# Kernel tuning notes

Measured on AMD Instinct MI355X. Metric: run time of the kernel, lower is better.

Reference implementation:

```python
import jax, jax.numpy as jnp
import numpy as np

NEG_LARGE = -2.0**32 + 1.0


def setup_inputs() -> dict:
    key = jax.random.key(0)
    ks = jax.random.split(key, 8)
    B, L, D = 2048, 200, 64  # D = embedding_dim, features are 2D wide
    H1, H2 = 80, 40
    queries = jax.random.normal(ks[0], (B, 2 * D), dtype=jnp.float32)
    user_behaviors = jax.random.normal(ks[1], (B, L, 2 * D), dtype=jnp.float32)
    masks = jax.random.randint(ks[2], (B, L), 0, 2, dtype=jnp.int32)
    s = 1.0 / np.sqrt(8 * D)
    w1 = jax.random.uniform(ks[3], (8 * D, H1), minval=-s, maxval=s, dtype=jnp.float32)
    b1 = jnp.zeros((H1,), jnp.float32)
    s2 = 1.0 / np.sqrt(H1)
    w2 = jax.random.uniform(ks[4], (H1, H2), minval=-s2, maxval=s2, dtype=jnp.float32)
    b2 = jnp.zeros((H2,), jnp.float32)
    s3 = 1.0 / np.sqrt(H2)
    w3 = jax.random.uniform(ks[5], (H2, 1), minval=-s3, maxval=s3, dtype=jnp.float32)
    b3 = jnp.zeros((1,), jnp.float32)
    return {"queries": queries, "user_behaviors": user_behaviors, "masks": masks,
            "w1": w1, "b1": b1, "w2": w2, "b2": b2, "w3": w3, "b3": b3}


def reference(queries, user_behaviors, masks, w1, b1, w2, b2, w3, b3):
    B, L, twoD = user_behaviors.shape
    q = jnp.broadcast_to(queries[:, None, :], (B, L, twoD))  # (B, L, 2D)
    feats = jnp.concatenate([q, user_behaviors, q - user_behaviors,
                             q * user_behaviors], axis=-1)  # (B, L, 8D)
    h = jax.nn.sigmoid(jnp.einsum('blf,fh->blh', feats, w1) + b1)
    h = jax.nn.sigmoid(jnp.einsum('blh,hk->blk', h, w2) + b2)
    scores = jnp.einsum('blk,ko->blo', h, w3) + b3  # (B, L, 1)
    valid = (masks != 0)[:, :, None]
    scores = jnp.where(valid, scores, NEG_LARGE)
    attn = jax.nn.softmax(scores, axis=1)  # (B, L, 1)
    return jnp.sum(attn * user_behaviors, axis=1)  # (B, 2D)
```

## Files before the change

### kernel.cpp

```cpp
#include <hip/hip_runtime.h>
#include <cstddef>


#define L_   200
#define D2_  128

typedef __attribute__((ext_vector_type(8))) short bf16x8;
typedef __attribute__((ext_vector_type(4))) float f32x4;
typedef __attribute__((ext_vector_type(4))) unsigned int u32x4;

union U8 { u32x4 u; bf16x8 b; };

__device__ __forceinline__ float sigmoidf_(float x) { return 1.0f / (1.0f + __expf(-x)); }

__device__ __forceinline__ unsigned int f2bf_(float x) {
  unsigned int u = __float_as_uint(x);
  return (u + 0x7fffu + ((u >> 16) & 1u)) >> 16;
}
__device__ __forceinline__ unsigned int pk2_(float a, float b) {
  return f2bf_(a) | (f2bf_(b) << 16);
}
__device__ __forceinline__ unsigned int pk2f_(float a, float b) {
  unsigned int r;
  asm("v_cvt_pk_bf16_f32 %0, %1, %2" : "=v"(r) : "v"(a), "v"(b));
  return r;
}

extern "C" __global__ void __launch_bounds__(128)
din_setup_kernel(const float* __restrict__ queries,
                 const float* __restrict__ w1,
                 const float* __restrict__ b1,
                 const float* __restrict__ w2,
                 float* __restrict__ qt,
                 float* __restrict__ wbc,
                 float* __restrict__ wd,
                 u32x4* __restrict__ w2a,
                 u32x4* __restrict__ w2b)
{
  const int bb = blockIdx.x;
  const int t  = threadIdx.x;

  if (bb < 8) {
    for (int s = bb * 160 + t; s < bb * 160 + 160; s += 128) {
      int nn = s & 15, kg = (s >> 4) & 3, g = s >> 6;
      int kc = g / 5, nt = g - kc * 5;
      int h = nt * 16 + nn, k0 = kc * 32 + kg * 8;
      #pragma unroll
      for (int j = 0; j < 8; ++j) {
        int k = k0 + j;
        wbc[s * 8 + j] = w1[(128 + k) * 80 + h] - w1[(256 + k) * 80 + h];
        wd [s * 8 + j] = w1[(384 + k) * 80 + h];
      }
    }
  } else if (bb == 8) {
    for (int s = t; s < 384; s += 128) {
      int nn = s & 15, g = s >> 4, nt2 = g >> 3, kg = g & 7;
      int j = nt2 * 16 + nn, k0 = kg * 8;
      u32x4 v = { 0u, 0u, 0u, 0u };
      if (j < 40) {
        float e0 = w2[(k0 + 0) * 40 + j], e1 = w2[(k0 + 1) * 40 + j];
        float e2 = w2[(k0 + 2) * 40 + j], e3 = w2[(k0 + 3) * 40 + j];
        float e4 = w2[(k0 + 4) * 40 + j], e5 = w2[(k0 + 5) * 40 + j];
        float e6 = w2[(k0 + 6) * 40 + j], e7 = w2[(k0 + 7) * 40 + j];
        v = (u32x4){ pk2_(e0, e1), pk2_(e2, e3), pk2_(e4, e5), pk2_(e6, e7) };
      }
      w2a[s] = v;
    }
    for (int s = t; s < 96; s += 128) {
      int nn = s & 15, g = s >> 4, nt2 = g >> 1, kgt = g & 1;
      int j = nt2 * 16 + nn, k0 = 64 + kgt * 8;
      u32x4 v = { 0u, 0u, 0u, 0u };
      if (j < 40) {
        float e0 = w2[(k0 + 0) * 40 + j], e1 = w2[(k0 + 1) * 40 + j];
        float e2 = w2[(k0 + 2) * 40 + j], e3 = w2[(k0 + 3) * 40 + j];
        float e4 = w2[(k0 + 4) * 40 + j], e5 = w2[(k0 + 5) * 40 + j];
        float e6 = w2[(k0 + 6) * 40 + j], e7 = w2[(k0 + 7) * 40 + j];
        v = (u32x4){ pk2_(e0, e1), pk2_(e2, e3), pk2_(e4, e5), pk2_(e6, e7) };
      }
      w2b[s] = v;
    }
  } else {
    const int b = bb - 9;
    __shared__ float qs[128];
    if (t < 128) qs[t] = queries[(size_t)b * D2_ + t];
    __syncthreads();
    if (t < 80) {
      float acc = b1[t];
      #pragma unroll 4
      for (int k = 0; k < 128; ++k)
        acc += qs[k] * (w1[k * 80 + t] + w1[(256 + k) * 80 + t]);
      qt[(size_t)b * 80 + t] = acc;
    }
  }
}

extern "C" __global__ void __launch_bounds__(256, 4)
din_scores_kernel(const float* __restrict__ queries,
                  const float* __restrict__ ub,
                  const float* __restrict__ b2,
                  const float* __restrict__ w3,
                  const float* __restrict__ qt,
                  const float* __restrict__ wbc,
                  const float* __restrict__ wd,
                  const u32x4* __restrict__ w2a,
                  const u32x4* __restrict__ w2b,
                  float* __restrict__ scores_ws)
{
  __shared__ __align__(16) char  pool[20480];
  __shared__ __align__(16) char  scratch[10240];
  __shared__ __align__(16) float qt_s[80];
  __shared__ __align__(16) float b2_s[48];
  __shared__ __align__(16) float w3_s[48];

  const int bc    = blockIdx.x;
  const int b     = bc >> 1;
  const int chunk = bc & 1;
  const int t     = threadIdx.x;
  const int wave  = t >> 6;
  const int lane  = t & 63;
  const int n16   = lane & 15;
  const int rg    = lane >> 4;

  const int st  = chunk ? (wave < 2 ? 7 + wave * 2 : 9 + wave) : wave * 2;
  const int cnt = chunk ? (wave < 2 ? 2 : 1) : (wave < 3 ? 2 : 1);

  const float* ubbase = ub + (size_t)b * (L_ * D2_);
  const float* qrow   = queries + (size_t)b * D2_;

  if (t < 80) qt_s[t] = qt[(size_t)b * 80 + t];
  if (t < 48) {
    b2_s[t] = (t < 40) ? b2[t] : 0.0f;
    w3_s[t] = (t < 40) ? w3[t] : 0.0f;
  }

  {
    u32x4* dst = (u32x4*)pool;
    const float4* wbc4 = (const float4*)wbc;
    const float4* wd4  = (const float4*)wd;
    #pragma unroll
    for (int i = 0; i < 5; ++i) {
      int s = i * 256 + t;
      int kg = (s >> 4) & 3, g = s >> 6;
      int kc = g / 5;
      int k0 = kc * 32 + kg * 8;
      float4 c0 = wbc4[2 * s], c1 = wbc4[2 * s + 1];
      float4 d0 = wd4 [2 * s], d1 = wd4 [2 * s + 1];
      float4 q0 = *(const float4*)(qrow + k0);
      float4 q1 = *(const float4*)(qrow + k0 + 4);
      dst[s] = (u32x4){ pk2f_(c0.x + q0.x * d0.x, c0.y + q0.y * d0.y),
                        pk2f_(c0.z + q0.z * d0.z, c0.w + q0.w * d0.w),
                        pk2f_(c1.x + q1.x * d1.x, c1.y + q1.y * d1.y),
                        pk2f_(c1.z + q1.z * d1.z, c1.w + q1.w * d1.w) };
    }
  }
  __syncthreads();

  const float* pa[2];
  #pragma unroll
  for (int i = 0; i < 2; ++i) {
    int row = (st + i) * 16 + n16;
    int rc  = (row < L_) ? row : (L_ - 1);
    pa[i] = ubbase + (size_t)rc * D2_ + rg * 8;
  }

  f32x4 acc[2][5];
  #pragma unroll
  for (int i = 0; i < 2; ++i)
    #pragma unroll
    for (int nt = 0; nt < 5; ++nt) acc[i][nt] = (f32x4){0.f, 0.f, 0.f, 0.f};

  const bf16x8* Bf = (const bf16x8*)pool;
  for (int kc = 0; kc < 4; ++kc) {
    U8 av[2];
    #pragma unroll
    for (int i = 0; i < 2; ++i) {
      if (i < cnt) {
        const float4* src = (const float4*)(pa[i] + kc * 32);
        float4 u0 = src[0], u1 = src[1];
        av[i].u = (u32x4){ pk2f_(u0.x, u0.y), pk2f_(u0.z, u0.w),
                           pk2f_(u1.x, u1.y), pk2f_(u1.z, u1.w) };
      }
    }
    #pragma unroll
    for (int nt = 0; nt < 5; ++nt) {
      bf16x8 bv = Bf[(kc * 5 + nt) * 64 + lane];
      #pragma unroll
      for (int i = 0; i < 2; ++i)
        if (i < cnt)
          acc[i][nt] = __builtin_amdgcn_mfma_f32_16x16x32_bf16(av[i].b, bv, acc[i][nt], 0, 0, 0);
    }
  }

  {
    unsigned short* hv  = (unsigned short*)(scratch + wave * 2560);
    const bf16x8*   hvf = (const bf16x8*)(scratch + wave * 2560);
    const bf16x8*   w2af = (const bf16x8*)w2a;
    const bf16x8*   w2bf = (const bf16x8*)w2b;

    for (int i = 0; i < 2; ++i) {
      if (i < cnt) {
        const int mt = st + i;

        #pragma unroll
        for (int nt = 0; nt < 5; ++nt) {
          int h  = nt * 16 + n16;
          int kg = h >> 3;
          float qtv = qt_s[h];
          #pragma unroll
          for (int r = 0; r < 4; ++r) {
            float x = acc[i][nt][r] + qtv;
            hv[(kg * 16 + rg * 4 + r) * 8 + (h & 7)] = (unsigned short)f2bf_(sigmoidf_(x));
          }
        }

        f32x4 acc2[3];
        #pragma unroll
        for (int n2 = 0; n2 < 3; ++n2) acc2[n2] = (f32x4){0.f, 0.f, 0.f, 0.f};

        #pragma unroll
        for (int ks = 0; ks < 2; ++ks) {
          bf16x8 av = hvf[(ks * 4 + rg) * 16 + n16];
          #pragma unroll
          for (int n2 = 0; n2 < 3; ++n2) {
            bf16x8 bv = w2af[(n2 * 8 + ks * 4 + rg) * 16 + n16];
            acc2[n2] = __builtin_amdgcn_mfma_f32_16x16x32_bf16(av, bv, acc2[n2], 0, 0, 0);
          }
        }
        {
          bf16x8 av = (bf16x8){0, 0, 0, 0, 0, 0, 0, 0};
          if (lane < 32) av = hvf[(8 + rg) * 16 + n16];
          #pragma unroll
          for (int n2 = 0; n2 < 3; ++n2) {
            bf16x8 bv = (bf16x8){0, 0, 0, 0, 0, 0, 0, 0};
            if (lane < 32) bv = w2bf[(n2 * 2 + rg) * 16 + n16];
            acc2[n2] = __builtin_amdgcn_mfma_f32_16x16x32_bf16(av, bv, acc2[n2], 0, 0, 0);
          }
        }

        #pragma unroll
        for (int r = 0; r < 4; ++r) {
          float s = 0.0f;
          #pragma unroll
          for (int n2 = 0; n2 < 3; ++n2) {
            int j = n2 * 16 + n16;
            s += sigmoidf_(acc2[n2][r] + b2_s[j]) * w3_s[j];
          }
          s += __shfl_xor(s, 1, 64);
          s += __shfl_xor(s, 2, 64);
          s += __shfl_xor(s, 4, 64);
          s += __shfl_xor(s, 8, 64);
          int l = mt * 16 + rg * 4 + r;
          if (n16 == 0 && l < L_) scores_ws[(size_t)b * L_ + l] = s;
        }
      }
    }
  }
}

extern "C" __global__ void __launch_bounds__(256, 4)
din_softmax_wsum_kernel(const float* __restrict__ ub,
                        const int*   __restrict__ masks,
                        const float* __restrict__ scores_ws,
                        float* __restrict__ out)
{
  __shared__ __align__(16) float scores_s[208];
  __shared__ __align__(16) float wsum_s[1088];
  __shared__ float red_s[8];

  const int b    = blockIdx.x;
  const int t    = threadIdx.x;
  const int wave = t >> 6;
  const int lane = t & 63;

  const float* ubbase = ub + (size_t)b * (L_ * D2_);

  float sval = -INFINITY;
  if (t < L_) {
    int   mv = masks[(size_t)b * L_ + t];
    float sc = scores_ws[(size_t)b * L_ + t];
    sval = mv ? sc : -4294967295.0f;
  }
  float m = sval;
  #pragma unroll
  for (int o = 32; o > 0; o >>= 1) m = fmaxf(m, __shfl_xor(m, o, 64));
  if (lane == 0) red_s[wave] = m;
  __syncthreads();
  m = fmaxf(fmaxf(red_s[0], red_s[1]), fmaxf(red_s[2], red_s[3]));
  float e = (t < L_) ? __expf(sval - m) : 0.0f;
  float ssum = e;
  #pragma unroll
  for (int o = 32; o > 0; o >>= 1) ssum += __shfl_xor(ssum, o, 64);
  if (lane == 0) red_s[4 + wave] = ssum;
  __syncthreads();
  ssum = red_s[4] + red_s[5] + red_s[6] + red_s[7];
  if (t < L_) scores_s[t] = e / ssum;
  __syncthreads();

  {
    const float4* ub4base = (const float4*)ubbase;
    int d4 = t & 31;
    int lg = t >> 5;
    float4 o = make_float4(0.f, 0.f, 0.f, 0.f);
    #pragma unroll
    for (int l = lg; l < L_; l += 8) {
      float w = scores_s[l];
      float4 v = ub4base[l * 32 + d4];
      o.x += w * v.x; o.y += w * v.y; o.z += w * v.z; o.w += w * v.w;
    }
    *(float4*)(wsum_s + lg * 136 + d4 * 4) = o;
    __syncthreads();
    if (t < 128) {
      float s = 0.0f;
      #pragma unroll
      for (int g = 0; g < 8; ++g) s += wsum_s[g * 136 + t];
      out[(size_t)b * 128 + t] = s;
    }
  }
}

extern "C" __global__ void __launch_bounds__(256, 4)
din_attn_fallback(const float* __restrict__ queries,
                  const float* __restrict__ ub,
                  const int*   __restrict__ masks,
                  const float* __restrict__ b2,
                  const float* __restrict__ w3,
                  const float* __restrict__ qt,
                  const float* __restrict__ wbc,
                  const float* __restrict__ wd,
                  const u32x4* __restrict__ w2a,
                  const u32x4* __restrict__ w2b,
                  float* __restrict__ out)
{
  __shared__ __align__(16) char  pool[33280];
  __shared__ __align__(16) float wsum_s[1088];
  __shared__ __align__(16) float qt_s[80];
  __shared__ __align__(16) float b2_s[48];
  __shared__ __align__(16) float w3_s[48];
  __shared__ __align__(16) float scores_s[208];
  __shared__ float red_s[8];

  const int b    = blockIdx.x;
  const int t    = threadIdx.x;
  const int wave = t >> 6;
  const int lane = t & 63;
  const int n16  = lane & 15;
  const int rg   = lane >> 4;

  const float* ubbase = ub + (size_t)b * (L_ * D2_);
  const float* qrow   = queries + (size_t)b * D2_;

  if (t < 80) qt_s[t] = qt[(size_t)b * 80 + t];
  if (t < 48) {
    b2_s[t] = (t < 40) ? b2[t] : 0.0f;
    w3_s[t] = (t < 40) ? w3[t] : 0.0f;
  }

  {
    u32x4* dst = (u32x4*)pool;
    const float4* wbc4 = (const float4*)wbc;
    const float4* wd4  = (const float4*)wd;
    #pragma unroll
    for (int i = 0; i < 5; ++i) {
      int s = i * 256 + t;
      int kg = (s >> 4) & 3, g = s >> 6;
      int kc = g / 5;
      int k0 = kc * 32 + kg * 8;
      float4 c0 = wbc4[2 * s], c1 = wbc4[2 * s + 1];
      float4 d0 = wd4 [2 * s], d1 = wd4 [2 * s + 1];
      float4 q0 = *(const float4*)(qrow + k0);
      float4 q1 = *(const float4*)(qrow + k0 + 4);
      dst[s] = (u32x4){ pk2f_(c0.x + q0.x * d0.x, c0.y + q0.y * d0.y),
                        pk2f_(c0.z + q0.z * d0.z, c0.w + q0.w * d0.w),
                        pk2f_(c1.x + q1.x * d1.x, c1.y + q1.y * d1.y),
                        pk2f_(c1.z + q1.z * d1.z, c1.w + q1.w * d1.w) };
    }
  }
  __syncthreads();

  f32x4 acc[4][5];
  #pragma unroll
  for (int i = 0; i < 4; ++i)
    #pragma unroll
    for (int nt = 0; nt < 5; ++nt) acc[i][nt] = (f32x4){0.f, 0.f, 0.f, 0.f};

  const bf16x8* Bf = (const bf16x8*)pool;
  for (int kc = 0; kc < 4; ++kc) {
    bf16x8 bvv[5];
    #pragma unroll
    for (int nt = 0; nt < 5; ++nt) bvv[nt] = Bf[(kc * 5 + nt) * 64 + lane];
    #pragma unroll
    for (int i = 0; i < 4; ++i) {
      int mt = wave + i * 4;
      if (mt < 13) {
        int row = mt * 16 + n16;
        float4 u0 = make_float4(0.f, 0.f, 0.f, 0.f);
        float4 u1 = make_float4(0.f, 0.f, 0.f, 0.f);
        if (row < L_) {
          const float4* src = (const float4*)(ubbase + (size_t)row * D2_ + kc * 32 + rg * 8);
          u0 = src[0]; u1 = src[1];
        }
        U8 av;
        av.u = (u32x4){ pk2f_(u0.x, u0.y), pk2f_(u0.z, u0.w),
                        pk2f_(u1.x, u1.y), pk2f_(u1.z, u1.w) };
        #pragma unroll
        for (int nt = 0; nt < 5; ++nt)
          acc[i][nt] = __builtin_amdgcn_mfma_f32_16x16x32_bf16(av.b, bvv[nt], acc[i][nt], 0, 0, 0);
      }
    }
  }
  __syncthreads();

  {
    unsigned short* hv = (unsigned short*)pool;
    #pragma unroll
    for (int i = 0; i < 4; ++i) {
      int mt = wave + i * 4;
      if (mt < 13) {
        #pragma unroll
        for (int nt = 0; nt < 5; ++nt) {
          int h = nt * 16 + n16;
          float qtv = qt_s[h];
          int kg = h >> 3;
          int slotbase = (kg < 8) ? (mt * 8 + kg) : (1664 + mt * 2 + (kg - 8));
          #pragma unroll
          for (int r = 0; r < 4; ++r) {
            float x = acc[i][nt][r] + qtv;
            hv[(slotbase * 16 + rg * 4 + r) * 8 + (h & 7)] =
                (unsigned short)f2bf_(sigmoidf_(x));
          }
        }
      }
    }
  }

  {
    const bf16x8* hvf  = (const bf16x8*)pool;
    const bf16x8* w2af = (const bf16x8*)w2a;
    const bf16x8* w2bf = (const bf16x8*)w2b;
    #pragma unroll
    for (int i = 0; i < 4; ++i) {
      int mt = wave + i * 4;
      if (mt < 13) {
        f32x4 acc2[3];
        #pragma unroll
        for (int n2 = 0; n2 < 3; ++n2) acc2[n2] = (f32x4){0.f, 0.f, 0.f, 0.f};
        #pragma unroll
        for (int ks = 0; ks < 2; ++ks) {
          bf16x8 av = hvf[(mt * 8 + ks * 4 + rg) * 16 + n16];
          #pragma unroll
          for (int n2 = 0; n2 < 3; ++n2) {
            bf16x8 bv = w2af[(n2 * 8 + ks * 4 + rg) * 16 + n16];
            acc2[n2] = __builtin_amdgcn_mfma_f32_16x16x32_bf16(av, bv, acc2[n2], 0, 0, 0);
          }
        }
        {
          bf16x8 av = (bf16x8){0, 0, 0, 0, 0, 0, 0, 0};
          if (lane < 32) av = hvf[(1664 + mt * 2 + rg) * 16 + n16];
          #pragma unroll
          for (int n2 = 0; n2 < 3; ++n2) {
            bf16x8 bv = (bf16x8){0, 0, 0, 0, 0, 0, 0, 0};
            if (lane < 32) bv = w2bf[(n2 * 2 + rg) * 16 + n16];
            acc2[n2] = __builtin_amdgcn_mfma_f32_16x16x32_bf16(av, bv, acc2[n2], 0, 0, 0);
          }
        }
        #pragma unroll
        for (int r = 0; r < 4; ++r) {
          float s = 0.0f;
          #pragma unroll
          for (int n2 = 0; n2 < 3; ++n2) {
            int j = n2 * 16 + n16;
            s += sigmoidf_(acc2[n2][r] + b2_s[j]) * w3_s[j];
          }
          s += __shfl_xor(s, 1, 64);
          s += __shfl_xor(s, 2, 64);
          s += __shfl_xor(s, 4, 64);
          s += __shfl_xor(s, 8, 64);
          int l = mt * 16 + rg * 4 + r;
          if (n16 == 0 && l < L_) scores_s[l] = s;
        }
      }
    }
  }
  __syncthreads();

  float sval = -INFINITY;
  if (t < L_) {
    int mv = masks[(size_t)b * L_ + t];
    sval = mv ? scores_s[t] : -4294967295.0f;
  }
  float m = sval;
  #pragma unroll
  for (int o = 32; o > 0; o >>= 1) m = fmaxf(m, __shfl_xor(m, o, 64));
  if (lane == 0) red_s[wave] = m;
  __syncthreads();
  m = fmaxf(fmaxf(red_s[0], red_s[1]), fmaxf(red_s[2], red_s[3]));
  float e = (t < L_) ? __expf(sval - m) : 0.0f;
  float ssum = e;
  #pragma unroll
  for (int o = 32; o > 0; o >>= 1) ssum += __shfl_xor(ssum, o, 64);
  if (lane == 0) red_s[4 + wave] = ssum;
  __syncthreads();
  ssum = red_s[4] + red_s[5] + red_s[6] + red_s[7];
  if (t < L_) scores_s[t] = e / ssum;
  __syncthreads();

  {
    const float4* ub4base = (const float4*)ubbase;
    int d4 = t & 31;
    int lg = t >> 5;
    float4 o = make_float4(0.f, 0.f, 0.f, 0.f);
    #pragma unroll
    for (int l = lg; l < L_; l += 8) {
      float w = scores_s[l];
      float4 v = ub4base[l * 32 + d4];
      o.x += w * v.x; o.y += w * v.y; o.z += w * v.z; o.w += w * v.w;
    }
    *(float4*)(wsum_s + lg * 136 + d4 * 4) = o;
    __syncthreads();
    if (t < 128) {
      float s = 0.0f;
      #pragma unroll
      for (int g = 0; g < 8; ++g) s += wsum_s[g * 136 + t];
      out[(size_t)b * 128 + t] = s;
    }
  }
}

extern "C" void kernel_launch(void* const* d_in, const int* in_sizes, int n_in,
                              void* d_out, int out_size, void* d_ws, size_t ws_size,
                              hipStream_t stream) {
  const float* queries = (const float*)d_in[0];
  const float* ub      = (const float*)d_in[1];
  const int*   masks   = (const int*)d_in[2];
  const float* w1      = (const float*)d_in[3];
  const float* b1      = (const float*)d_in[4];
  const float* w2      = (const float*)d_in[5];
  const float* b2      = (const float*)d_in[6];
  const float* w3      = (const float*)d_in[7];
  float* out = (float*)d_out;

  const int B = in_sizes[0] / D2_;

  char*  ws  = (char*)d_ws;
  float* qt  = (float*)ws;
  float* wbc = (float*)(ws + (size_t)B * 320);
  float* wd  = (float*)(ws + (size_t)B * 320 + 40960);
  u32x4* w2a = (u32x4*)(ws + (size_t)B * 320 + 81920);
  u32x4* w2b = (u32x4*)(ws + (size_t)B * 320 + 88064);
  size_t sc_off = (size_t)B * 320 + 90112;
  float* scores = (float*)(ws + sc_off);
  size_t need = sc_off + (size_t)B * L_ * 4;

  din_setup_kernel<<<B + 9, 128, 0, stream>>>(queries, w1, b1, w2, qt, wbc, wd, w2a, w2b);

  if (ws_size >= need) {
    din_scores_kernel<<<2 * B, 256, 0, stream>>>(queries, ub, b2, w3,
                                                 qt, wbc, wd, w2a, w2b, scores);
    din_softmax_wsum_kernel<<<B, 256, 0, stream>>>(ub, masks, scores, out);
  } else {
    din_attn_fallback<<<B, 256, 0, stream>>>(queries, ub, masks, b2, w3,
                                             qt, wbc, wd, w2a, w2b, out);
  }
}
```

Before: 375.0 us.

## Precompute per-batch bf16 query-folded W1 in setup kernel, read from global in scores

The setup kernel now builds, for each batch row, the query-dependent bf16 B-matrix for the first layer (W_b - W_c + q*W_d) in the MFMA fragment layout and writes it to workspace. The scores kernel loads those fragments straight from global instead of rebuilding them in LDS. It also keeps qt, b2 and w3 in registers rather than shared memory, which removes the LDS staging and the block barrier. The cost is about 20 KB of extra workspace writes and reads per batch row, plus heavier per-row work in the setup kernel.

Result: slower. 408.8 us (+9.0%).

```diff
diff --git a/kernel.cpp b/kernel.cpp
--- a/kernel.cpp
+++ b/kernel.cpp
@@ -24,6 +24,279 @@
   unsigned int r;
   asm("v_cvt_pk_bf16_f32 %0, %1, %2" : "=v"(r) : "v"(a), "v"(b));
   return r;
+}
+
+extern "C" __global__ void __launch_bounds__(256)
+din_setup2_kernel(const float* __restrict__ queries,
+                  const float* __restrict__ w1,
+                  const float* __restrict__ b1,
+                  const float* __restrict__ w2,
+                  float* __restrict__ qt,
+                  u32x4* __restrict__ w2a,
+                  u32x4* __restrict__ w2b,
+                  u32x4* __restrict__ bwq)
+{
+  const int bb = blockIdx.x;
+  const int t  = threadIdx.x;
+
+  if (bb == (int)gridDim.x - 1) {
+    for (int s = t; s < 384; s += 256) {
+      int nn = s & 15, g = s >> 4, nt2 = g >> 3, kg = g & 7;
+      int j = nt2 * 16 + nn, k0 = kg * 8;
+      u32x4 v = { 0u, 0u, 0u, 0u };
+      if (j < 40) {
+        float e0 = w2[(k0 + 0) * 40 + j], e1 = w2[(k0 + 1) * 40 + j];
+        float e2 = w2[(k0 + 2) * 40 + j], e3 = w2[(k0 + 3) * 40 + j];
+        float e4 = w2[(k0 + 4) * 40 + j], e5 = w2[(k0 + 5) * 40 + j];
+        float e6 = w2[(k0 + 6) * 40 + j], e7 = w2[(k0 + 7) * 40 + j];
+        v = (u32x4){ pk2_(e0, e1), pk2_(e2, e3), pk2_(e4, e5), pk2_(e6, e7) };
+      }
+      w2a[s] = v;
+    }
+    for (int s = t; s < 96; s += 256) {
+      int nn = s & 15, g = s >> 4, nt2 = g >> 1, kgt = g & 1;
+      int j = nt2 * 16 + nn, k0 = 64 + kgt * 8;
+      u32x4 v = { 0u, 0u, 0u, 0u };
+      if (j < 40) {
+        float e0 = w2[(k0 + 0) * 40 + j], e1 = w2[(k0 + 1) * 40 + j];
+        float e2 = w2[(k0 + 2) * 40 + j], e3 = w2[(k0 + 3) * 40 + j];
+        float e4 = w2[(k0 + 4) * 40 + j], e5 = w2[(k0 + 5) * 40 + j];
+        float e6 = w2[(k0 + 6) * 40 + j], e7 = w2[(k0 + 7) * 40 + j];
+        v = (u32x4){ pk2_(e0, e1), pk2_(e2, e3), pk2_(e4, e5), pk2_(e6, e7) };
+      }
+      w2b[s] = v;
+    }
+    return;
+  }
+
+  const int b = bb;
+  __shared__ float qs[128];
+  if (t < 128) qs[t] = queries[(size_t)b * D2_ + t];
+  __syncthreads();
+
+  if (t < 80) {
+    float acc = b1[t];
+    #pragma unroll 4
+    for (int k = 0; k < 128; ++k)
+      acc += qs[k] * (w1[k * 80 + t] + w1[(256 + k) * 80 + t]);
+    qt[(size_t)b * 80 + t] = acc;
+  }
+
+  u32x4* dst = bwq + (size_t)b * 1280;
+  #pragma unroll
+  for (int i = 0; i < 5; ++i) {
+    int s = i * 256 + t;
+    int nn = s & 15, kg = (s >> 4) & 3, g = s >> 6;
+    int kc = g / 5, nt = g - kc * 5;
+    int h = nt * 16 + nn, k0 = kc * 32 + kg * 8;
+    float wv[8];
+    #pragma unroll
+    for (int j = 0; j < 8; ++j) {
+      int k = k0 + j;
+      wv[j] = (w1[(128 + k) * 80 + h] - w1[(256 + k) * 80 + h])
+            + qs[k] * w1[(384 + k) * 80 + h];
+    }
+    dst[s] = (u32x4){ pk2f_(wv[0], wv[1]), pk2f_(wv[2], wv[3]),
+                      pk2f_(wv[4], wv[5]), pk2f_(wv[6], wv[7]) };
+  }
+}
+
+extern "C" __global__ void __launch_bounds__(256, 4)
+din_scores2_kernel(const float* __restrict__ ub,
+                   const float* __restrict__ b2,
+                   const float* __restrict__ w3,
+                   const float* __restrict__ qt,
+                   const u32x4* __restrict__ bwq,
+                   const u32x4* __restrict__ w2a,
+                   const u32x4* __restrict__ w2b,
+                   float* __restrict__ scores_ws)
+{
+  __shared__ __align__(16) char scratch[10240];
+
+  const int bc    = blockIdx.x;
+  const int b     = bc >> 1;
+  const int chunk = bc & 1;
+  const int t     = threadIdx.x;
+  const int wave  = t >> 6;
+  const int lane  = t & 63;
+  const int n16   = lane & 15;
+  const int rg    = lane >> 4;
+
+  const int st  = chunk ? (wave < 2 ? 7 + wave * 2 : 9 + wave) : wave * 2;
+  const int cnt = chunk ? (wave < 2 ? 2 : 1) : (wave < 3 ? 2 : 1);
+
+  const float* ubbase = ub + (size_t)b * (L_ * D2_);
+
+  float qtv[5], b2v[3], w3v[3];
+  #pragma unroll
+  for (int nt = 0; nt < 5; ++nt) qtv[nt] = qt[(size_t)b * 80 + nt * 16 + n16];
+  #pragma unroll
+  for (int n2 = 0; n2 < 3; ++n2) {
+    int j = n2 * 16 + n16;
+    int jc = (j < 40) ? j : 0;
+    b2v[n2] = b2[jc];
+    w3v[n2] = (j < 40) ? w3[jc] : 0.0f;
+  }
+
+  const float* pa[2];
+  #pragma unroll
+  for (int i = 0; i < 2; ++i) {
+    int row = (st + i) * 16 + n16;
+    int rc  = (row < L_) ? row : (L_ - 1);
+    pa[i] = ubbase + (size_t)rc * D2_ + rg * 8;
+  }
+
+  f32x4 acc[2][5];
+  #pragma unroll
+  for (int i = 0; i < 2; ++i)
+    #pragma unroll
+    for (int nt = 0; nt < 5; ++nt) acc[i][nt] = (f32x4){0.f, 0.f, 0.f, 0.f};
+
+  const u32x4* bq = bwq + (size_t)b * 1280;
+  for (int kc = 0; kc < 4; ++kc) {
+    U8 av[2];
+    #pragma unroll
+    for (int i = 0; i < 2; ++i) {
+      if (i < cnt) {
+        const float4* src = (const float4*)(pa[i] + kc * 32);
+        float4 u0 = src[0], u1 = src[1];
+        av[i].u = (u32x4){ pk2f_(u0.x, u0.y), pk2f_(u0.z, u0.w),
+                           pk2f_(u1.x, u1.y), pk2f_(u1.z, u1.w) };
+      }
+    }
+    #pragma unroll
+    for (int nt = 0; nt < 5; ++nt) {
+      U8 bv;
+      bv.u = bq[(kc * 5 + nt) * 64 + lane];
+      #pragma unroll
+      for (int i = 0; i < 2; ++i)
+        if (i < cnt)
+          acc[i][nt] = __builtin_amdgcn_mfma_f32_16x16x32_bf16(av[i].b, bv.b, acc[i][nt], 0, 0, 0);
+    }
+  }
+
+  {
+    unsigned short* hv  = (unsigned short*)(scratch + wave * 2560);
+    const bf16x8*   hvf = (const bf16x8*)(scratch + wave * 2560);
+    const bf16x8*   w2af = (const bf16x8*)w2a;
+    const bf16x8*   w2bf = (const bf16x8*)w2b;
+
+    for (int i = 0; i < 2; ++i) {
+      if (i < cnt) {
+        const int mt = st + i;
+
+        #pragma unroll
+        for (int nt = 0; nt < 5; ++nt) {
+          int h  = nt * 16 + n16;
+          int kg = h >> 3;
+          #pragma unroll
+          for (int r = 0; r < 4; ++r) {
+            float x = acc[i][nt][r] + qtv[nt];
+            hv[(kg * 16 + rg * 4 + r) * 8 + (h & 7)] = (unsigned short)f2bf_(sigmoidf_(x));
+          }
+        }
+
+        f32x4 acc2[3];
+        #pragma unroll
+        for (int n2 = 0; n2 < 3; ++n2) acc2[n2] = (f32x4){0.f, 0.f, 0.f, 0.f};
+
+        #pragma unroll
+        for (int ks = 0; ks < 2; ++ks) {
+          bf16x8 av = hvf[(ks * 4 + rg) * 16 + n16];
+          #pragma unroll
+          for (int n2 = 0; n2 < 3; ++n2) {
+            bf16x8 bv = w2af[(n2 * 8 + ks * 4 + rg) * 16 + n16];
+            acc2[n2] = __builtin_amdgcn_mfma_f32_16x16x32_bf16(av, bv, acc2[n2], 0, 0, 0);
+          }
+        }
+        {
+          bf16x8 av = (bf16x8){0, 0, 0, 0, 0, 0, 0, 0};
+          if (lane < 32) av = hvf[(8 + rg) * 16 + n16];
+          #pragma unroll
+          for (int n2 = 0; n2 < 3; ++n2) {
+            bf16x8 bv = (bf16x8){0, 0, 0, 0, 0, 0, 0, 0};
+            if (lane < 32) bv = w2bf[(n2 * 2 + rg) * 16 + n16];
+            acc2[n2] = __builtin_amdgcn_mfma_f32_16x16x32_bf16(av, bv, acc2[n2], 0, 0, 0);
+          }
+        }
+
+        #pragma unroll
+        for (int r = 0; r < 4; ++r) {
+          float s = 0.0f;
+          #pragma unroll
+          for (int n2 = 0; n2 < 3; ++n2)
+            s += sigmoidf_(acc2[n2][r] + b2v[n2]) * w3v[n2];
+          s += __shfl_xor(s, 1, 64);
+          s += __shfl_xor(s, 2, 64);
+          s += __shfl_xor(s, 4, 64);
+          s += __shfl_xor(s, 8, 64);
+          int l = mt * 16 + rg * 4 + r;
+          if (n16 == 0 && l < L_) scores_ws[(size_t)b * L_ + l] = s;
+        }
+      }
+    }
+  }
+}
+
+extern "C" __global__ void __launch_bounds__(256, 4)
+din_softmax_wsum_kernel(const float* __restrict__ ub,
+                        const int*   __restrict__ masks,
+                        const float* __restrict__ scores_ws,
+                        float* __restrict__ out)
+{
+  __shared__ __align__(16) float scores_s[208];
+  __shared__ __align__(16) float wsum_s[1088];
+  __shared__ float red_s[8];
+
+  const int b    = blockIdx.x;
+  const int t    = threadIdx.x;
+  const int wave = t >> 6;
+  const int lane = t & 63;
+
+  const float* ubbase = ub + (size_t)b * (L_ * D2_);
+
+  float sval = -INFINITY;
+  if (t < L_) {
+    int   mv = masks[(size_t)b * L_ + t];
+    float sc = scores_ws[(size_t)b * L_ + t];
+    sval = mv ? sc : -4294967295.0f;
+  }
+  float m = sval;
+  #pragma unroll
+  for (int o = 32; o > 0; o >>= 1) m = fmaxf(m, __shfl_xor(m, o, 64));
+  if (lane == 0) red_s[wave] = m;
+  __syncthreads();
+  m = fmaxf(fmaxf(red_s[0], red_s[1]), fmaxf(red_s[2], red_s[3]));
+  float e = (t < L_) ? __expf(sval - m) : 0.0f;
+  float ssum = e;
+  #pragma unroll
+  for (int o = 32; o > 0; o >>= 1) ssum += __shfl_xor(ssum, o, 64);
+  if (lane == 0) red_s[4 + wave] = ssum;
+  __syncthreads();
+  ssum = red_s[4] + red_s[5] + red_s[6] + red_s[7];
+  if (t < L_) scores_s[t] = e / ssum;
+  __syncthreads();
+
+  {
+    const float4* ub4base = (const float4*)ubbase;
+    int d4 = t & 31;
+    int lg = t >> 5;
+    float4 o = make_float4(0.f, 0.f, 0.f, 0.f);
+    #pragma unroll
+    for (int l = lg; l < L_; l += 8) {
+      float w = scores_s[l];
+      float4 v = ub4base[l * 32 + d4];
+      o.x += w * v.x; o.y += w * v.y; o.z += w * v.z; o.w += w * v.w;
+    }
+    *(float4*)(wsum_s + lg * 136 + d4 * 4) = o;
+    __syncthreads();
+    if (t < 128) {
+      float s = 0.0f;
+      #pragma unroll
+      for (int g = 0; g < 8; ++g) s += wsum_s[g * 136 + t];
+      out[(size_t)b * 128 + t] = s;
+    }
+  }
 }
 
 extern "C" __global__ void __launch_bounds__(128)
@@ -90,230 +363,6 @@
       for (int k = 0; k < 128; ++k)
         acc += qs[k] * (w1[k * 80 + t] + w1[(256 + k) * 80 + t]);
       qt[(size_t)b * 80 + t] = acc;
-    }
-  }
-}
-
-extern "C" __global__ void __launch_bounds__(256, 4)
-din_scores_kernel(const float* __restrict__ queries,
-                  const float* __restrict__ ub,
-                  const float* __restrict__ b2,
-                  const float* __restrict__ w3,
-                  const float* __restrict__ qt,
-                  const float* __restrict__ wbc,
-                  const float* __restrict__ wd,
-                  const u32x4* __restrict__ w2a,
-                  const u32x4* __restrict__ w2b,
-                  float* __restrict__ scores_ws)
-{
-  __shared__ __align__(16) char  pool[20480];
-  __shared__ __align__(16) char  scratch[10240];
-  __shared__ __align__(16) float qt_s[80];
-  __shared__ __align__(16) float b2_s[48];
-  __shared__ __align__(16) float w3_s[48];
-
-  const int bc    = blockIdx.x;
-  const int b     = bc >> 1;
-  const int chunk = bc & 1;
-  const int t     = threadIdx.x;
-  const int wave  = t >> 6;
-  const int lane  = t & 63;
-  const int n16   = lane & 15;
-  const int rg    = lane >> 4;
-
-  const int st  = chunk ? (wave < 2 ? 7 + wave * 2 : 9 + wave) : wave * 2;
-  const int cnt = chunk ? (wave < 2 ? 2 : 1) : (wave < 3 ? 2 : 1);
-
-  const float* ubbase = ub + (size_t)b * (L_ * D2_);
-  const float* qrow   = queries + (size_t)b * D2_;
-
-  if (t < 80) qt_s[t] = qt[(size_t)b * 80 + t];
-  if (t < 48) {
-    b2_s[t] = (t < 40) ? b2[t] : 0.0f;
-    w3_s[t] = (t < 40) ? w3[t] : 0.0f;
-  }
-
-  {
-    u32x4* dst = (u32x4*)pool;
-    const float4* wbc4 = (const float4*)wbc;
-    const float4* wd4  = (const float4*)wd;
-    #pragma unroll
-    for (int i = 0; i < 5; ++i) {
-      int s = i * 256 + t;
-      int kg = (s >> 4) & 3, g = s >> 6;
-      int kc = g / 5;
-      int k0 = kc * 32 + kg * 8;
-      float4 c0 = wbc4[2 * s], c1 = wbc4[2 * s + 1];
-      float4 d0 = wd4 [2 * s], d1 = wd4 [2 * s + 1];
-      float4 q0 = *(const float4*)(qrow + k0);
-      float4 q1 = *(const float4*)(qrow + k0 + 4);
-      dst[s] = (u32x4){ pk2f_(c0.x + q0.x * d0.x, c0.y + q0.y * d0.y),
-                        pk2f_(c0.z + q0.z * d0.z, c0.w + q0.w * d0.w),
-                        pk2f_(c1.x + q1.x * d1.x, c1.y + q1.y * d1.y),
-                        pk2f_(c1.z + q1.z * d1.z, c1.w + q1.w * d1.w) };
-    }
-  }
-  __syncthreads();
-
-  const float* pa[2];
-  #pragma unroll
-  for (int i = 0; i < 2; ++i) {
-    int row = (st + i) * 16 + n16;
-    int rc  = (row < L_) ? row : (L_ - 1);
-    pa[i] = ubbase + (size_t)rc * D2_ + rg * 8;
-  }
-
-  f32x4 acc[2][5];
-  #pragma unroll
-  for (int i = 0; i < 2; ++i)
-    #pragma unroll
-    for (int nt = 0; nt < 5; ++nt) acc[i][nt] = (f32x4){0.f, 0.f, 0.f, 0.f};
-
-  const bf16x8* Bf = (const bf16x8*)pool;
-  for (int kc = 0; kc < 4; ++kc) {
-    U8 av[2];
-    #pragma unroll
-    for (int i = 0; i < 2; ++i) {
-      if (i < cnt) {
-        const float4* src = (const float4*)(pa[i] + kc * 32);
-        float4 u0 = src[0], u1 = src[1];
-        av[i].u = (u32x4){ pk2f_(u0.x, u0.y), pk2f_(u0.z, u0.w),
-                           pk2f_(u1.x, u1.y), pk2f_(u1.z, u1.w) };
-      }
-    }
-    #pragma unroll
-    for (int nt = 0; nt < 5; ++nt) {
-      bf16x8 bv = Bf[(kc * 5 + nt) * 64 + lane];
-      #pragma unroll
-      for (int i = 0; i < 2; ++i)
-        if (i < cnt)
-          acc[i][nt] = __builtin_amdgcn_mfma_f32_16x16x32_bf16(av[i].b, bv, acc[i][nt], 0, 0, 0);
-    }
-  }
-
-  {
-    unsigned short* hv  = (unsigned short*)(scratch + wave * 2560);
-    const bf16x8*   hvf = (const bf16x8*)(scratch + wave * 2560);
-    const bf16x8*   w2af = (const bf16x8*)w2a;
-    const bf16x8*   w2bf = (const bf16x8*)w2b;
-
-    for (int i = 0; i < 2; ++i) {
-      if (i < cnt) {
-        const int mt = st + i;
-
-        #pragma unroll
-        for (int nt = 0; nt < 5; ++nt) {
-          int h  = nt * 16 + n16;
-          int kg = h >> 3;
-          float qtv = qt_s[h];
-          #pragma unroll
-          for (int r = 0; r < 4; ++r) {
-            float x = acc[i][nt][r] + qtv;
-            hv[(kg * 16 + rg * 4 + r) * 8 + (h & 7)] = (unsigned short)f2bf_(sigmoidf_(x));
-          }
-        }
-
-        f32x4 acc2[3];
-        #pragma unroll
-        for (int n2 = 0; n2 < 3; ++n2) acc2[n2] = (f32x4){0.f, 0.f, 0.f, 0.f};
-
-        #pragma unroll
-        for (int ks = 0; ks < 2; ++ks) {
-          bf16x8 av = hvf[(ks * 4 + rg) * 16 + n16];
-          #pragma unroll
-          for (int n2 = 0; n2 < 3; ++n2) {
-            bf16x8 bv = w2af[(n2 * 8 + ks * 4 + rg) * 16 + n16];
-            acc2[n2] = __builtin_amdgcn_mfma_f32_16x16x32_bf16(av, bv, acc2[n2], 0, 0, 0);
-          }
-        }
-        {
-          bf16x8 av = (bf16x8){0, 0, 0, 0, 0, 0, 0, 0};
-          if (lane < 32) av = hvf[(8 + rg) * 16 + n16];
-          #pragma unroll
-          for (int n2 = 0; n2 < 3; ++n2) {
-            bf16x8 bv = (bf16x8){0, 0, 0, 0, 0, 0, 0, 0};
-            if (lane < 32) bv = w2bf[(n2 * 2 + rg) * 16 + n16];
-            acc2[n2] = __builtin_amdgcn_mfma_f32_16x16x32_bf16(av, bv, acc2[n2], 0, 0, 0);
-          }
-        }
-
-        #pragma unroll
-        for (int r = 0; r < 4; ++r) {
-          float s = 0.0f;
-          #pragma unroll
-          for (int n2 = 0; n2 < 3; ++n2) {
-            int j = n2 * 16 + n16;
-            s += sigmoidf_(acc2[n2][r] + b2_s[j]) * w3_s[j];
-          }
-          s += __shfl_xor(s, 1, 64);
-          s += __shfl_xor(s, 2, 64);
-          s += __shfl_xor(s, 4, 64);
-          s += __shfl_xor(s, 8, 64);
-          int l = mt * 16 + rg * 4 + r;
-          if (n16 == 0 && l < L_) scores_ws[(size_t)b * L_ + l] = s;
-        }
-      }
-    }
-  }
-}
-
-extern "C" __global__ void __launch_bounds__(256, 4)
-din_softmax_wsum_kernel(const float* __restrict__ ub,
-                        const int*   __restrict__ masks,
-                        const float* __restrict__ scores_ws,
-                        float* __restrict__ out)
-{
-  __shared__ __align__(16) float scores_s[208];
-  __shared__ __align__(16) float wsum_s[1088];
-  __shared__ float red_s[8];
-
-  const int b    = blockIdx.x;
-  const int t    = threadIdx.x;
-  const int wave = t >> 6;
-  const int lane = t & 63;
-
-  const float* ubbase = ub + (size_t)b * (L_ * D2_);
-
-  float sval = -INFINITY;
-  if (t < L_) {
-    int   mv = masks[(size_t)b * L_ + t];
-    float sc = scores_ws[(size_t)b * L_ + t];
-    sval = mv ? sc : -4294967295.0f;
-  }
-  float m = sval;
-  #pragma unroll
-  for (int o = 32; o > 0; o >>= 1) m = fmaxf(m, __shfl_xor(m, o, 64));
-  if (lane == 0) red_s[wave] = m;
-  __syncthreads();
-  m = fmaxf(fmaxf(red_s[0], red_s[1]), fmaxf(red_s[2], red_s[3]));
-  float e = (t < L_) ? __expf(sval - m) : 0.0f;
-  float ssum = e;
-  #pragma unroll
-  for (int o = 32; o > 0; o >>= 1) ssum += __shfl_xor(ssum, o, 64);
-  if (lane == 0) red_s[4 + wave] = ssum;
-  __syncthreads();
-  ssum = red_s[4] + red_s[5] + red_s[6] + red_s[7];
-  if (t < L_) scores_s[t] = e / ssum;
-  __syncthreads();
-
-  {
-    const float4* ub4base = (const float4*)ubbase;
-    int d4 = t & 31;
-    int lg = t >> 5;
-    float4 o = make_float4(0.f, 0.f, 0.f, 0.f);
-    #pragma unroll
-    for (int l = lg; l < L_; l += 8) {
-      float w = scores_s[l];
-      float4 v = ub4base[l * 32 + d4];
-      o.x += w * v.x; o.y += w * v.y; o.z += w * v.z; o.w += w * v.w;
-    }
-    *(float4*)(wsum_s + lg * 136 + d4 * 4) = o;
-    __syncthreads();
-    if (t < 128) {
-      float s = 0.0f;
-      #pragma unroll
-      for (int g = 0; g < 8; ++g) s += wsum_s[g * 136 + t];
-      out[(size_t)b * 128 + t] = s;
     }
   }
 }
@@ -541,23 +590,32 @@
 
   const int B = in_sizes[0] / D2_;
 
-  char*  ws  = (char*)d_ws;
-  float* qt  = (float*)ws;
-  float* wbc = (float*)(ws + (size_t)B * 320);
-  float* wd  = (float*)(ws + (size_t)B * 320 + 40960);
-  u32x4* w2a = (u32x4*)(ws + (size_t)B * 320 + 81920);
-  u32x4* w2b = (u32x4*)(ws + (size_t)B * 320 + 88064);
-  size_t sc_off = (size_t)B * 320 + 90112;
-  float* scores = (float*)(ws + sc_off);
-  size_t need = sc_off + (size_t)B * L_ * 4;
-
-  din_setup_kernel<<<B + 9, 128, 0, stream>>>(queries, w1, b1, w2, qt, wbc, wd, w2a, w2b);
-
-  if (ws_size >= need) {
-    din_scores_kernel<<<2 * B, 256, 0, stream>>>(queries, ub, b2, w3,
-                                                 qt, wbc, wd, w2a, w2b, scores);
+  char* ws = (char*)d_ws;
+
+  size_t off_qt  = 0;
+  size_t off_w2a = (size_t)B * 320;
+  size_t off_w2b = off_w2a + 6144;
+  size_t off_sc  = off_w2b + 1536 + 512;
+  size_t off_bwq = off_sc + (size_t)B * 800;
+  size_t need_fast = off_bwq + (size_t)B * 20480;
+
+  if (ws_size >= need_fast) {
+    float* qt     = (float*)(ws + off_qt);
+    u32x4* w2a    = (u32x4*)(ws + off_w2a);
+    u32x4* w2b    = (u32x4*)(ws + off_w2b);
+    float* scores = (float*)(ws + off_sc);
+    u32x4* bwq    = (u32x4*)(ws + off_bwq);
+
+    din_setup2_kernel<<<B + 1, 256, 0, stream>>>(queries, w1, b1, w2, qt, w2a, w2b, bwq);
+    din_scores2_kernel<<<2 * B, 256, 0, stream>>>(ub, b2, w3, qt, bwq, w2a, w2b, scores);
     din_softmax_wsum_kernel<<<B, 256, 0, stream>>>(ub, masks, scores, out);
   } else {
+    float* qt  = (float*)ws;
+    float* wbc = (float*)(ws + (size_t)B * 320);
+    float* wd  = (float*)(ws + (size_t)B * 320 + 40960);
+    u32x4* w2a = (u32x4*)(ws + (size_t)B * 320 + 81920);
+    u32x4* w2b = (u32x4*)(ws + (size_t)B * 320 + 88064);
+    din_setup_kernel<<<B + 9, 128, 0, stream>>>(queries, w1, b1, w2, qt, wbc, wd, w2a, w2b);
     din_attn_fallback<<<B, 256, 0, stream>>>(queries, ub, masks, b2, w3,
                                              qt, wbc, wd, w2a, w2b, out);
   }
```
